# Kernel optimization log

Hardware: AMD Instinct MI355X
Metric: run time of the kernel (lower is better)

The kernel has to match this reference:

```python
import jax, jax.numpy as jnp
import numpy as np

BATCH = 256
SEQ = 2048        # sequences (in_features of each per-channel Linear)
C = 32            # input_size (number of independent channels/layers)
EMB = 2048        # embedding_dim (out_features)


def setup_inputs() -> dict:
    key = jax.random.key(0)
    kx, kw, kb = jax.random.split(key, 3)
    x = jax.random.normal(kx, (BATCH, SEQ, C), dtype=jnp.float32)
    # PyTorch nn.Linear init: U(-1/sqrt(fan_in), 1/sqrt(fan_in))
    bound = 1.0 / np.sqrt(SEQ)
    W = jax.random.uniform(kw, (C, SEQ, EMB), minval=-bound, maxval=bound, dtype=jnp.float32)
    b = jax.random.uniform(kb, (C, EMB), minval=-bound, maxval=bound, dtype=jnp.float32)
    return {"x": x, "W": W, "b": b}


def reference(x, W, b):
    # x: (B, S, C) -> transpose to (B, C, S); per-channel Linear + ReLU.
    # Grouped GEMM: out[b,c,e] = relu(sum_s x[b,s,c] * W[c,s,e] + b[c,e])
    xc = jnp.transpose(x, (0, 2, 1))                 # (B, C, S)
    out = jnp.einsum('bcs,cse->bce', xc, W) + b      # (B, C, E)
    return jax.nn.relu(out)
```

## Files before the change

### kernel.cpp

```cpp
#include <hip/hip_runtime.h>

#define BATCH 256
#define SEQ   2048
#define NC    32
#define EMB   2048
#define NT    32

typedef unsigned short ushort_t;
using f32x4  = __attribute__((ext_vector_type(4))) float;
using bf16x8 = __attribute__((ext_vector_type(8))) short;

using u32_gl = __attribute__((address_space(1))) const unsigned int;
using u32_ld = __attribute__((address_space(3))) unsigned int;

__device__ __forceinline__ unsigned int f2bf(float f) {
  unsigned int u = __float_as_uint(f);
  u += 0x7FFFu + ((u >> 16) & 1u);
  return u >> 16;
}

#define SB() __builtin_amdgcn_sched_barrier(0)

__global__ __launch_bounds__(256) void transpose_x_kernel(
    const float* __restrict__ x, ushort_t* __restrict__ xT) {
  __shared__ float tile[64][33];
  const int b  = blockIdx.x >> 5;
  const int st = blockIdx.x & 31;
  const int t  = threadIdx.x;
  const float* src = x + ((size_t)b * SEQ + (size_t)st * 64) * NC;
#pragma unroll
  for (int i = 0; i < 2; ++i) {
    int idx = t + i * 256;
    float4 v = reinterpret_cast<const float4*>(src)[idx];
    int s = idx >> 3;
    int c = (idx & 7) * 4;
    tile[s][c + 0] = v.x; tile[s][c + 1] = v.y;
    tile[s][c + 2] = v.z; tile[s][c + 3] = v.w;
  }
  __syncthreads();
  const int c  = t >> 3;
  const int si = (t & 7) * 8;
  unsigned int q[4];
#pragma unroll
  for (int p = 0; p < 4; ++p) {
    unsigned int h0 = f2bf(tile[si + 2 * p + 0][c]);
    unsigned int h1 = f2bf(tile[si + 2 * p + 1][c]);
    q[p] = h0 | (h1 << 16);
  }
  ushort_t* dst = xT + (size_t)c * (BATCH * SEQ) + (size_t)b * SEQ + st * 64 + si;
  *reinterpret_cast<uint4*>(dst) = make_uint4(q[0], q[1], q[2], q[3]);
}

template <int PB, int Q3>
__device__ __forceinline__ void gemm_iter(
    int t, const ushort_t* __restrict__ xTc, const float* __restrict__ Wc,
    char* Alds, char* Blds, f32x4 (&wv)[2][4], f32x4 (&acc)[4][4],
    int tid, int wr, int wc, int g, int lm, int e0) {
  constexpr int QS = (Q3 + 2) % 3;
  const int srow4 = tid >> 5;
  const int e4    = tid & 31;

  asm volatile("s_waitcnt vmcnt(12)" ::: "memory");

#pragma unroll
  for (int i = 0; i < 4; ++i) {
    const int e_local = e4 * 4 + i;
    unsigned int q0 = f2bf(wv[PB][0][i]) | (f2bf(wv[PB][1][i]) << 16);
    unsigned int q1 = f2bf(wv[PB][2][i]) | (f2bf(wv[PB][3][i]) << 16);
    int byte = (e_local * 128 + srow4 * 8) ^ ((e_local & 7) << 4);
    *reinterpret_cast<uint2*>(Blds + PB * 16384 + byte) = make_uint2(q0, q1);
  }

  {
    const int tn = (t + 2) & (NT - 1);
    const float* wp = Wc + (size_t)(tn * 64 + srow4 * 4) * EMB + e0 + e4 * 4;
#pragma unroll
    for (int r = 0; r < 4; ++r)
      wv[PB][r] = *reinterpret_cast<const f32x4*>(wp + (size_t)r * EMB);
  }
  SB();

  asm volatile("s_waitcnt lgkmcnt(0)" ::: "memory");
  __builtin_amdgcn_s_barrier();

  {
    const int s0n = ((t + 2) & (NT - 1)) * 64;
#pragma unroll
    for (int i = 0; i < 4; ++i) {
      int ch   = i * 512 + tid;
      int m    = ch >> 3;
      int slot = (ch & 7) ^ (m & 7);
      const ushort_t* src = xTc + (size_t)m * SEQ + s0n + slot * 8;
      __builtin_amdgcn_global_load_lds(
          (u32_gl*)src, (u32_ld*)(Alds + QS * 32768 + ch * 16), 16, 0, 0);
    }
  }

  asm volatile("s_waitcnt vmcnt(16)" ::: "memory");
  SB();

  __builtin_amdgcn_s_barrier();

#pragma unroll
  for (int ks = 0; ks < 2; ++ks) {
    bf16x8 af[4], bfr[4];
#pragma unroll
    for (int mi = 0; mi < 4; ++mi) {
      int m_local = wr * 64 + mi * 16 + lm;
      int byte = (m_local * 128 + (ks * 4 + g) * 16) ^ ((m_local & 7) << 4);
      af[mi] = *reinterpret_cast<const bf16x8*>(Alds + Q3 * 32768 + byte);
    }
#pragma unroll
    for (int ni = 0; ni < 4; ++ni) {
      int e_local = wc * 64 + ni * 16 + lm;
      int byte = (e_local * 128 + (ks * 4 + g) * 16) ^ ((e_local & 7) << 4);
      bfr[ni] = *reinterpret_cast<const bf16x8*>(Blds + PB * 16384 + byte);
    }
#pragma unroll
    for (int mi = 0; mi < 4; ++mi)
#pragma unroll
      for (int ni = 0; ni < 4; ++ni)
        acc[mi][ni] = __builtin_amdgcn_mfma_f32_16x16x32_bf16(
            af[mi], bfr[ni], acc[mi][ni], 0, 0, 0);
  }
}

__global__ __launch_bounds__(512, 2) void grouped_gemm_pipe(
    const ushort_t* __restrict__ xT,
    const float* __restrict__ W,
    const float* __restrict__ bias,
    float* __restrict__ out) {
  __shared__ ushort_t AldsU[3][256 * 64];
  __shared__ ushort_t BldsU[2][128 * 64];

  const int bid = (blockIdx.x & 7) * 64 + (blockIdx.x >> 3);
  const int c   = bid >> 4;
  const int et  = bid & 15;
  const int e0  = et * 128;

  const int tid  = threadIdx.x;
  const int w    = tid >> 6;
  const int wr   = w >> 1;
  const int wc   = w & 1;
  const int lane = tid & 63;
  const int g    = lane >> 4;
  const int lm   = lane & 15;

  const float* Wc = W + (size_t)c * SEQ * EMB;
  const ushort_t* xTc = xT + (size_t)c * (BATCH * SEQ);
  char* Alds = (char*)&AldsU[0][0];
  char* Blds = (char*)&BldsU[0][0];

  f32x4 wv[2][4];
  f32x4 acc[4][4];
#pragma unroll
  for (int i = 0; i < 4; ++i)
#pragma unroll
    for (int j = 0; j < 4; ++j) acc[i][j] = (f32x4){0.f, 0.f, 0.f, 0.f};

  {
    const int srow4 = tid >> 5;
    const int e4    = tid & 31;
    const float* wp = Wc + (size_t)(srow4 * 4) * EMB + e0 + e4 * 4;
#pragma unroll
    for (int r = 0; r < 4; ++r)
      wv[0][r] = *reinterpret_cast<const f32x4*>(wp + (size_t)r * EMB);
    SB();
#pragma unroll
    for (int i = 0; i < 4; ++i) {
      int ch   = i * 512 + tid;
      int m    = ch >> 3;
      int slot = (ch & 7) ^ (m & 7);
      const ushort_t* src = xTc + (size_t)m * SEQ + slot * 8;
      __builtin_amdgcn_global_load_lds(
          (u32_gl*)src, (u32_ld*)(Alds + ch * 16), 16, 0, 0);
    }
    SB();
#pragma unroll
    for (int r = 0; r < 4; ++r)
      wv[1][r] = *reinterpret_cast<const f32x4*>(wp + (size_t)(64 + r) * EMB);
    SB();
#pragma unroll
    for (int i = 0; i < 4; ++i) {
      int ch   = i * 512 + tid;
      int m    = ch >> 3;
      int slot = (ch & 7) ^ (m & 7);
      const ushort_t* src = xTc + (size_t)m * SEQ + 64 + slot * 8;
      __builtin_amdgcn_global_load_lds(
          (u32_gl*)src, (u32_ld*)(Alds + 32768 + ch * 16), 16, 0, 0);
    }
    SB();
  }

  for (int t = 0; t < 30; t += 6) {
    gemm_iter<0, 0>(t,     xTc, Wc, Alds, Blds, wv, acc, tid, wr, wc, g, lm, e0);
    gemm_iter<1, 1>(t + 1, xTc, Wc, Alds, Blds, wv, acc, tid, wr, wc, g, lm, e0);
    gemm_iter<0, 2>(t + 2, xTc, Wc, Alds, Blds, wv, acc, tid, wr, wc, g, lm, e0);
    gemm_iter<1, 0>(t + 3, xTc, Wc, Alds, Blds, wv, acc, tid, wr, wc, g, lm, e0);
    gemm_iter<0, 1>(t + 4, xTc, Wc, Alds, Blds, wv, acc, tid, wr, wc, g, lm, e0);
    gemm_iter<1, 2>(t + 5, xTc, Wc, Alds, Blds, wv, acc, tid, wr, wc, g, lm, e0);
  }
  gemm_iter<0, 0>(30, xTc, Wc, Alds, Blds, wv, acc, tid, wr, wc, g, lm, e0);
  gemm_iter<1, 1>(31, xTc, Wc, Alds, Blds, wv, acc, tid, wr, wc, g, lm, e0);

  asm volatile("s_waitcnt vmcnt(0)" ::: "memory");

  const float* bc = bias + (size_t)c * EMB;
#pragma unroll
  for (int ni = 0; ni < 4; ++ni) {
    const int e = e0 + wc * 64 + ni * 16 + lm;
    const float bv = bc[e];
#pragma unroll
    for (int mi = 0; mi < 4; ++mi) {
      f32x4 a = acc[mi][ni];
      const int mbase = wr * 64 + mi * 16 + g * 4;
#pragma unroll
      for (int r = 0; r < 4; ++r) {
        float v = a[r] + bv;
        v = fmaxf(v, 0.f);
        out[((size_t)(mbase + r) * NC + c) * EMB + e] = v;
      }
    }
  }
}

__global__ __launch_bounds__(256, 2) void grouped_gemm_fallback(
    const float* __restrict__ x, const float* __restrict__ W,
    const float* __restrict__ bias, float* __restrict__ out) {
  __shared__ ushort_t Alds[128 * 64];
  __shared__ ushort_t Blds[128 * 64];
  const int bid = blockIdx.x;
  const int c   = bid >> 5;
  const int et  = (bid >> 1) & 15;
  const int bt  = bid & 1;
  const int b0  = bt * 128;
  const int e0  = et * 128;
  const int tid  = threadIdx.x;
  const int w    = tid >> 6;
  const int wr   = w >> 1;
  const int wc   = w & 1;
  const int lane = tid & 63;
  const int g    = lane >> 4;
  const int lm   = lane & 15;
  const float* Wc = W + (size_t)c * SEQ * EMB;
  const int srow8 = tid >> 5;
  const int e4    = tid & 31;
  f32x4 acc[4][4];
#pragma unroll
  for (int i = 0; i < 4; ++i)
#pragma unroll
    for (int j = 0; j < 4; ++j) acc[i][j] = (f32x4){0.f, 0.f, 0.f, 0.f};
  for (int s0 = 0; s0 < SEQ; s0 += 64) {
#pragma unroll
    for (int i = 0; i < 4; ++i) {
      int ch   = i * 256 + tid;
      int m    = ch >> 3;
      int slot = (ch & 7) ^ (m & 7);
      const float* src = x + (size_t)(b0 + m) * (SEQ * NC)
                           + (size_t)(s0 + slot * 8) * NC + c;
      unsigned int q[4];
#pragma unroll
      for (int p = 0; p < 4; ++p) {
        unsigned int h0 = f2bf(src[(2 * p + 0) * NC]);
        unsigned int h1 = f2bf(src[(2 * p + 1) * NC]);
        q[p] = h0 | (h1 << 16);
      }
      *reinterpret_cast<uint4*>((char*)&Alds[0] + ch * 16) =
          make_uint4(q[0], q[1], q[2], q[3]);
    }
    {
      const float* wp = Wc + (size_t)(s0 + srow8 * 8) * EMB + e0 + e4 * 4;
      f32x4 wvv[8];
#pragma unroll
      for (int r = 0; r < 8; ++r)
        wvv[r] = *reinterpret_cast<const f32x4*>(wp + (size_t)r * EMB);
#pragma unroll
      for (int i = 0; i < 4; ++i) {
        const int e_local = e4 * 4 + i;
        unsigned int q0 = f2bf(wvv[0][i]) | (f2bf(wvv[1][i]) << 16);
        unsigned int q1 = f2bf(wvv[2][i]) | (f2bf(wvv[3][i]) << 16);
        unsigned int q2 = f2bf(wvv[4][i]) | (f2bf(wvv[5][i]) << 16);
        unsigned int q3 = f2bf(wvv[6][i]) | (f2bf(wvv[7][i]) << 16);
        int byte = (e_local * 128 + srow8 * 16) ^ ((e_local & 7) << 4);
        *reinterpret_cast<uint4*>((char*)&Blds[0] + byte) =
            make_uint4(q0, q1, q2, q3);
      }
    }
    __syncthreads();
#pragma unroll
    for (int ks = 0; ks < 2; ++ks) {
      bf16x8 af[4], bfr[4];
#pragma unroll
      for (int mi = 0; mi < 4; ++mi) {
        int m_local = wr * 64 + mi * 16 + lm;
        int byte = (m_local * 128 + (ks * 4 + g) * 16) ^ ((m_local & 7) << 4);
        af[mi] = *reinterpret_cast<const bf16x8*>((const char*)&Alds[0] + byte);
      }
#pragma unroll
      for (int ni = 0; ni < 4; ++ni) {
        int e_local = wc * 64 + ni * 16 + lm;
        int byte = (e_local * 128 + (ks * 4 + g) * 16) ^ ((e_local & 7) << 4);
        bfr[ni] = *reinterpret_cast<const bf16x8*>((const char*)&Blds[0] + byte);
      }
#pragma unroll
      for (int mi = 0; mi < 4; ++mi)
#pragma unroll
        for (int ni = 0; ni < 4; ++ni)
          acc[mi][ni] = __builtin_amdgcn_mfma_f32_16x16x32_bf16(
              af[mi], bfr[ni], acc[mi][ni], 0, 0, 0);
    }
    __syncthreads();
  }
  const float* bc = bias + (size_t)c * EMB;
#pragma unroll
  for (int ni = 0; ni < 4; ++ni) {
    const int e = e0 + wc * 64 + ni * 16 + lm;
    const float bv = bc[e];
#pragma unroll
    for (int mi = 0; mi < 4; ++mi) {
      f32x4 a = acc[mi][ni];
      const int mbase = b0 + wr * 64 + mi * 16 + g * 4;
#pragma unroll
      for (int r = 0; r < 4; ++r) {
        float v = a[r] + bv;
        v = fmaxf(v, 0.f);
        out[((size_t)(mbase + r) * NC + c) * EMB + e] = v;
      }
    }
  }
}

extern "C" void kernel_launch(void* const* d_in, const int* in_sizes, int n_in,
                              void* d_out, int out_size, void* d_ws, size_t ws_size,
                              hipStream_t stream) {
  const float* x    = (const float*)d_in[0];
  const float* W    = (const float*)d_in[1];
  const float* bias = (const float*)d_in[2];
  float* out        = (float*)d_out;

  const size_t xT_bytes = (size_t)NC * BATCH * SEQ * sizeof(ushort_t);

  if (ws_size >= xT_bytes) {
    ushort_t* xT = (ushort_t*)d_ws;
    transpose_x_kernel<<<BATCH * (SEQ / 64), 256, 0, stream>>>(x, xT);
    grouped_gemm_pipe<<<NC * (EMB / 128), 512, 0, stream>>>(xT, W, bias, out);
  } else {
    grouped_gemm_fallback<<<NC * 2 * (EMB / 128), 256, 0, stream>>>(x, W, bias, out);
  }
}
```

Measured before the change: 159.9 us.

## Shorten prefetch pipeline to distance one with nontemporal scalar W loads

The A-tile pipeline drops from a triple buffer with prefetch distance two to a double buffer with distance one. W is now fetched as 16 scalar nontemporal loads per thread in a strided pattern, issued at the start of each iteration, rather than four f32x4 loads, and the prologue no longer preloads the second tile. The output stores become nontemporal. This reduces LDS use, which may help occupancy, and keeps streaming data from polluting the cache, but latency hiding gets shallower and there are more, narrower load instructions.

```diff
diff --git a/kernel.cpp b/kernel.cpp
--- a/kernel.cpp
+++ b/kernel.cpp
@@ -51,40 +51,41 @@
   *reinterpret_cast<uint4*>(dst) = make_uint4(q[0], q[1], q[2], q[3]);
 }
 
-template <int PB, int Q3>
+template <int P>
 __device__ __forceinline__ void gemm_iter(
     int t, const ushort_t* __restrict__ xTc, const float* __restrict__ Wc,
-    char* Alds, char* Blds, f32x4 (&wv)[2][4], f32x4 (&acc)[4][4],
+    char* Alds, char* Blds, float (&wvs)[2][16], f32x4 (&acc)[4][4],
     int tid, int wr, int wc, int g, int lm, int e0) {
-  constexpr int QS = (Q3 + 2) % 3;
   const int srow4 = tid >> 5;
   const int e4    = tid & 31;
 
-  asm volatile("s_waitcnt vmcnt(12)" ::: "memory");
+  {
+    const int tn = (t + 1) & (NT - 1);
+    const float* wp = Wc + (size_t)(tn * 64 + srow4 * 4) * EMB + e0 + e4;
+#pragma unroll
+    for (int r = 0; r < 4; ++r)
+#pragma unroll
+      for (int i = 0; i < 4; ++i)
+        wvs[P ^ 1][r * 4 + i] =
+            __builtin_nontemporal_load(wp + (size_t)r * EMB + 32 * i);
+  }
+  SB();
+
+  asm volatile("s_waitcnt vmcnt(20)" ::: "memory");
 
 #pragma unroll
   for (int i = 0; i < 4; ++i) {
-    const int e_local = e4 * 4 + i;
-    unsigned int q0 = f2bf(wv[PB][0][i]) | (f2bf(wv[PB][1][i]) << 16);
-    unsigned int q1 = f2bf(wv[PB][2][i]) | (f2bf(wv[PB][3][i]) << 16);
+    const int e_local = e4 + 32 * i;
+    unsigned int lo = f2bf(wvs[P][0 * 4 + i]) | (f2bf(wvs[P][1 * 4 + i]) << 16);
+    unsigned int hi = f2bf(wvs[P][2 * 4 + i]) | (f2bf(wvs[P][3 * 4 + i]) << 16);
     int byte = (e_local * 128 + srow4 * 8) ^ ((e_local & 7) << 4);
-    *reinterpret_cast<uint2*>(Blds + PB * 16384 + byte) = make_uint2(q0, q1);
-  }
-
-  {
-    const int tn = (t + 2) & (NT - 1);
-    const float* wp = Wc + (size_t)(tn * 64 + srow4 * 4) * EMB + e0 + e4 * 4;
-#pragma unroll
-    for (int r = 0; r < 4; ++r)
-      wv[PB][r] = *reinterpret_cast<const f32x4*>(wp + (size_t)r * EMB);
-  }
-  SB();
-
+    *reinterpret_cast<uint2*>(Blds + P * 16384 + byte) = make_uint2(lo, hi);
+  }
   asm volatile("s_waitcnt lgkmcnt(0)" ::: "memory");
   __builtin_amdgcn_s_barrier();
 
   {
-    const int s0n = ((t + 2) & (NT - 1)) * 64;
+    const int s0n = ((t + 1) & (NT - 1)) * 64;
 #pragma unroll
     for (int i = 0; i < 4; ++i) {
       int ch   = i * 512 + tid;
@@ -92,11 +93,11 @@
       int slot = (ch & 7) ^ (m & 7);
       const ushort_t* src = xTc + (size_t)m * SEQ + s0n + slot * 8;
       __builtin_amdgcn_global_load_lds(
-          (u32_gl*)src, (u32_ld*)(Alds + QS * 32768 + ch * 16), 16, 0, 0);
-    }
-  }
-
-  asm volatile("s_waitcnt vmcnt(16)" ::: "memory");
+          (u32_gl*)src, (u32_ld*)(Alds + (P ^ 1) * 32768 + ch * 16), 16, 0, 0);
+    }
+  }
+
+  asm volatile("s_waitcnt vmcnt(20)" ::: "memory");
   SB();
 
   __builtin_amdgcn_s_barrier();
@@ -108,13 +109,13 @@
     for (int mi = 0; mi < 4; ++mi) {
       int m_local = wr * 64 + mi * 16 + lm;
       int byte = (m_local * 128 + (ks * 4 + g) * 16) ^ ((m_local & 7) << 4);
-      af[mi] = *reinterpret_cast<const bf16x8*>(Alds + Q3 * 32768 + byte);
+      af[mi] = *reinterpret_cast<const bf16x8*>(Alds + P * 32768 + byte);
     }
 #pragma unroll
     for (int ni = 0; ni < 4; ++ni) {
       int e_local = wc * 64 + ni * 16 + lm;
       int byte = (e_local * 128 + (ks * 4 + g) * 16) ^ ((e_local & 7) << 4);
-      bfr[ni] = *reinterpret_cast<const bf16x8*>(Blds + PB * 16384 + byte);
+      bfr[ni] = *reinterpret_cast<const bf16x8*>(Blds + P * 16384 + byte);
     }
 #pragma unroll
     for (int mi = 0; mi < 4; ++mi)
@@ -130,7 +131,7 @@
     const float* __restrict__ W,
     const float* __restrict__ bias,
     float* __restrict__ out) {
-  __shared__ ushort_t AldsU[3][256 * 64];
+  __shared__ ushort_t AldsU[2][256 * 64];
   __shared__ ushort_t BldsU[2][128 * 64];
 
   const int bid = (blockIdx.x & 7) * 64 + (blockIdx.x >> 3);
@@ -151,7 +152,7 @@
   char* Alds = (char*)&AldsU[0][0];
   char* Blds = (char*)&BldsU[0][0];
 
-  f32x4 wv[2][4];
+  float wvs[2][16];
   f32x4 acc[4][4];
 #pragma unroll
   for (int i = 0; i < 4; ++i)
@@ -161,10 +162,13 @@
   {
     const int srow4 = tid >> 5;
     const int e4    = tid & 31;
-    const float* wp = Wc + (size_t)(srow4 * 4) * EMB + e0 + e4 * 4;
+    const float* wp = Wc + (size_t)(srow4 * 4) * EMB + e0 + e4;
 #pragma unroll
     for (int r = 0; r < 4; ++r)
-      wv[0][r] = *reinterpret_cast<const f32x4*>(wp + (size_t)r * EMB);
+#pragma unroll
+      for (int i = 0; i < 4; ++i)
+        wvs[0][r * 4 + i] =
+            __builtin_nontemporal_load(wp + (size_t)r * EMB + 32 * i);
     SB();
 #pragma unroll
     for (int i = 0; i < 4; ++i) {
@@ -176,32 +180,12 @@
           (u32_gl*)src, (u32_ld*)(Alds + ch * 16), 16, 0, 0);
     }
     SB();
-#pragma unroll
-    for (int r = 0; r < 4; ++r)
-      wv[1][r] = *reinterpret_cast<const f32x4*>(wp + (size_t)(64 + r) * EMB);
-    SB();
-#pragma unroll
-    for (int i = 0; i < 4; ++i) {
-      int ch   = i * 512 + tid;
-      int m    = ch >> 3;
-      int slot = (ch & 7) ^ (m & 7);
-      const ushort_t* src = xTc + (size_t)m * SEQ + 64 + slot * 8;
-      __builtin_amdgcn_global_load_lds(
-          (u32_gl*)src, (u32_ld*)(Alds + 32768 + ch * 16), 16, 0, 0);
-    }
-    SB();
-  }
-
-  for (int t = 0; t < 30; t += 6) {
-    gemm_iter<0, 0>(t,     xTc, Wc, Alds, Blds, wv, acc, tid, wr, wc, g, lm, e0);
-    gemm_iter<1, 1>(t + 1, xTc, Wc, Alds, Blds, wv, acc, tid, wr, wc, g, lm, e0);
-    gemm_iter<0, 2>(t + 2, xTc, Wc, Alds, Blds, wv, acc, tid, wr, wc, g, lm, e0);
-    gemm_iter<1, 0>(t + 3, xTc, Wc, Alds, Blds, wv, acc, tid, wr, wc, g, lm, e0);
-    gemm_iter<0, 1>(t + 4, xTc, Wc, Alds, Blds, wv, acc, tid, wr, wc, g, lm, e0);
-    gemm_iter<1, 2>(t + 5, xTc, Wc, Alds, Blds, wv, acc, tid, wr, wc, g, lm, e0);
-  }
-  gemm_iter<0, 0>(30, xTc, Wc, Alds, Blds, wv, acc, tid, wr, wc, g, lm, e0);
-  gemm_iter<1, 1>(31, xTc, Wc, Alds, Blds, wv, acc, tid, wr, wc, g, lm, e0);
+  }
+
+  for (int t = 0; t < NT; t += 2) {
+    gemm_iter<0>(t,     xTc, Wc, Alds, Blds, wvs, acc, tid, wr, wc, g, lm, e0);
+    gemm_iter<1>(t + 1, xTc, Wc, Alds, Blds, wvs, acc, tid, wr, wc, g, lm, e0);
+  }
 
   asm volatile("s_waitcnt vmcnt(0)" ::: "memory");
 
@@ -218,7 +202,8 @@
       for (int r = 0; r < 4; ++r) {
         float v = a[r] + bv;
         v = fmaxf(v, 0.f);
-        out[((size_t)(mbase + r) * NC + c) * EMB + e] = v;
+        __builtin_nontemporal_store(
+            v, out + ((size_t)(mbase + r) * NC + c) * EMB + e);
       }
     }
   }
```

Measured after the change: 148.7 us. 1.07x faster.
